# Kernel tuning notes

Hardware: AMD Instinct MI355X
Metric: run time of the kernel (lower is better)

Reference implementation:

```python
import jax, jax.numpy as jnp
import numpy as np

NEG_SLOPE = 0.01  # torch LeakyReLU default
BN_EPS = 1e-5

def leaky_relu(x):
    return jnp.where(x >= 0, x, NEG_SLOPE * x)

def setup_inputs() -> dict:
    key = jax.random.key(0)
    kx, kw, k1w, k1b, k2w, k2b = jax.random.split(key, 6)
    B, S, d = 512, 256, 64
    H, E = 64, 8  # n_hidden_sets, n_elements
    X = jax.random.normal(kx, (B, S, d), dtype=jnp.float32)
    # Wc ~ U(-1, 1) per init_weights
    Wc = jax.random.uniform(kw, (d, H * E), dtype=jnp.float32, minval=-1.0, maxval=1.0)
    # Linear layers: torch default init ~ U(-1/sqrt(fan_in), 1/sqrt(fan_in))
    b1 = 1.0 / np.sqrt(H)
    fc1_w = jax.random.uniform(k1w, (32, H), dtype=jnp.float32, minval=-b1, maxval=b1)
    fc1_b = jax.random.uniform(k1b, (32,), dtype=jnp.float32, minval=-b1, maxval=b1)
    b2 = 1.0 / np.sqrt(32)
    fc2_w = jax.random.uniform(k2w, (1, 32), dtype=jnp.float32, minval=-b2, maxval=b2)
    fc2_b = jax.random.uniform(jax.random.fold_in(key, 7), (1,), dtype=jnp.float32, minval=-b2, maxval=b2)
    gamma = jnp.ones((32,), dtype=jnp.float32)
    beta = jnp.zeros((32,), dtype=jnp.float32)
    return {"X": X, "Wc": Wc, "fc1_w": fc1_w, "fc1_b": fc1_b,
            "gamma": gamma, "beta": beta, "fc2_w": fc2_w, "fc2_b": fc2_b}

def reference(X, Wc, fc1_w, fc1_b, gamma, beta, fc2_w, fc2_b):
    B, S, d = X.shape
    HE = Wc.shape[1]
    H = fc1_w.shape[1]          # n_hidden_sets
    E = HE // H                 # n_elements
    # [B,S,d] @ [d,H*E] -> [B,S,H*E], LeakyReLU epilogue
    t = leaky_relu(jnp.matmul(X, Wc))
    # torch .view: row-major reshape to [B,S,E,H]
    t = t.reshape(B, S, E, H)
    t = jnp.max(t, axis=2)      # max over elements -> [B,S,H]
    t = jnp.sum(t, axis=1)      # sum over set -> [B,H]
    # fc1
    t = t @ fc1_w.T + fc1_b     # [B,32]
    # BatchNorm1d, training-mode batch statistics (biased var)
    mu = jnp.mean(t, axis=0)
    var = jnp.mean(jnp.square(t - mu), axis=0)
    t = (t - mu) * jax.lax.rsqrt(var + BN_EPS) * gamma + beta
    t = leaky_relu(t)
    out = t @ fc2_w.T + fc2_b   # [B,1]
    return out[:, 0]
```

## Files before the change

kernel.cpp:

```cpp
#include <hip/hip_runtime.h>

typedef __bf16 bf16x4 __attribute__((ext_vector_type(4)));
typedef __bf16 bf16x8 __attribute__((ext_vector_type(8)));
typedef float  f32x4  __attribute__((ext_vector_type(4)));

#define XS 68

__global__ __launch_bounds__(256, 2)
void fused_main(const float* __restrict__ X, const float* __restrict__ Wc,
                const float* __restrict__ fc1_w, const float* __restrict__ fc1_b,
                float* __restrict__ out1)
{
    __shared__ __bf16 xlds[64 * XS];
    __shared__ float  t0row[64];

    const int tid  = threadIdx.x;
    const int b    = blockIdx.x;
    const int wave = tid >> 6;
    const int lane = tid & 63;
    const int n    = lane & 15;
    const int q    = lane >> 4;

    const float4* xg = (const float4*)(X + (size_t)b * 256 * 64);

    float4 xv[4];
    #pragma unroll
    for (int i = 0; i < 4; ++i) xv[i] = xg[tid + i * 256];

    bf16x8 bf0[8], bf1[8];
    {
        const float* wbase = Wc + (q * 8) * 512 + wave * 16 + n;
        #pragma unroll
        for (int e = 0; e < 8; ++e) {
            const float* p = wbase + e * 64;
            #pragma unroll
            for (int j = 0; j < 8; ++j) {
                bf0[e][j] = (__bf16)p[j * 512];
                bf1[e][j] = (__bf16)p[(j + 32) * 512];
            }
        }
    }

    float hsum = 0.0f;

    for (int st = 0; st < 4; ++st) {
        #pragma unroll
        for (int i = 0; i < 4; ++i) {
            const int p = tid + i * 256;
            bf16x4 o;
            o[0] = (__bf16)xv[i].x; o[1] = (__bf16)xv[i].y;
            o[2] = (__bf16)xv[i].z; o[3] = (__bf16)xv[i].w;
            const int r = p >> 4, ck = p & 15;
            *(bf16x4*)&xlds[r * XS + ck * 4] = o;
        }
        __syncthreads();

        if (st < 3) {
            const float4* xgn = xg + (st + 1) * 1024;
            #pragma unroll
            for (int i = 0; i < 4; ++i) xv[i] = xgn[tid + i * 256];
        }

        bf16x8 a0[4], a1[4];
        #pragma unroll
        for (int t = 0; t < 4; ++t) {
            const int base = (t * 16 + n) * XS + q * 8;
            bf16x4 p0 = *(const bf16x4*)&xlds[base];
            bf16x4 p1 = *(const bf16x4*)&xlds[base + 4];
            bf16x4 p2 = *(const bf16x4*)&xlds[base + 32];
            bf16x4 p3 = *(const bf16x4*)&xlds[base + 36];
            a0[t] = __builtin_shufflevector(p0, p1, 0, 1, 2, 3, 4, 5, 6, 7);
            a1[t] = __builtin_shufflevector(p2, p3, 0, 1, 2, 3, 4, 5, 6, 7);
        }

        float rmax[4][4];
        #pragma unroll
        for (int t = 0; t < 4; ++t)
            #pragma unroll
            for (int r4 = 0; r4 < 4; ++r4) rmax[t][r4] = -3.0e38f;

        #pragma unroll
        for (int e = 0; e < 8; ++e) {
            #pragma unroll
            for (int t = 0; t < 4; ++t) {
                f32x4 acc = {0.f, 0.f, 0.f, 0.f};
                acc = __builtin_amdgcn_mfma_f32_16x16x32_bf16(a0[t], bf0[e], acc, 0, 0, 0);
                acc = __builtin_amdgcn_mfma_f32_16x16x32_bf16(a1[t], bf1[e], acc, 0, 0, 0);
                #pragma unroll
                for (int r4 = 0; r4 < 4; ++r4) {
                    rmax[t][r4] = fmaxf(rmax[t][r4], fmaxf(acc[r4], 0.01f * acc[r4]));
                }
            }
        }

        float s = 0.f;
        #pragma unroll
        for (int t = 0; t < 4; ++t)
            #pragma unroll
            for (int r4 = 0; r4 < 4; ++r4) s += rmax[t][r4];
        s += __shfl_xor(s, 16);
        s += __shfl_xor(s, 32);
        hsum += s;
        __syncthreads();
    }

    if (lane < 16) t0row[wave * 16 + lane] = hsum;
    __syncthreads();

    if (wave == 0) {
        const int j = lane & 31, half = lane >> 5;
        float p = 0.f;
        #pragma unroll
        for (int i = 0; i < 32; ++i)
            p += t0row[half * 32 + i] * fc1_w[j * 64 + half * 32 + i];
        p += __shfl_xor(p, 32);
        if (half == 0) out1[b * 32 + j] = p + fc1_b[j];
    }
}

__global__ __launch_bounds__(512)
void bn_fc2(const float* __restrict__ out1, const float* __restrict__ gamma,
            const float* __restrict__ beta, const float* __restrict__ fc2_w,
            const float* __restrict__ fc2_b, float* __restrict__ out)
{
    __shared__ float psum[16][32];
    __shared__ float psumsq[16][32];
    __shared__ float sa[32], sc[32];

    const int tid = threadIdx.x;
    const int j   = tid & 31;
    const int sl  = tid >> 5;

    float s = 0.f, ss = 0.f;
    #pragma unroll
    for (int i = 0; i < 32; ++i) {
        float v = out1[(sl * 32 + i) * 32 + j];
        s  += v;
        ss += v * v;
    }
    psum[sl][j]   = s;
    psumsq[sl][j] = ss;
    __syncthreads();

    if (tid < 32) {
        float S = 0.f, SS = 0.f;
        #pragma unroll
        for (int i = 0; i < 16; ++i) { S += psum[i][tid]; SS += psumsq[i][tid]; }
        const float mu  = S * (1.0f / 512.0f);
        const float var = SS * (1.0f / 512.0f) - mu * mu;
        const float rs  = rsqrtf(var + 1e-5f);
        const float a   = rs * gamma[tid];
        sa[tid] = a;
        sc[tid] = beta[tid] - mu * a;
    }
    __syncthreads();

    float acc = 0.f;
    #pragma unroll
    for (int jj = 0; jj < 32; ++jj) {
        float v = out1[tid * 32 + jj];
        float y = v * sa[jj] + sc[jj];
        y = fmaxf(y, 0.01f * y);
        acc += y * fc2_w[jj];
    }
    out[tid] = acc + fc2_b[0];
}

extern "C" void kernel_launch(void* const* d_in, const int* in_sizes, int n_in,
                              void* d_out, int out_size, void* d_ws, size_t ws_size,
                              hipStream_t stream) {
    const float* X      = (const float*)d_in[0];
    const float* Wc     = (const float*)d_in[1];
    const float* fc1_w  = (const float*)d_in[2];
    const float* fc1_b  = (const float*)d_in[3];
    const float* gamma  = (const float*)d_in[4];
    const float* beta   = (const float*)d_in[5];
    const float* fc2_w  = (const float*)d_in[6];
    const float* fc2_b  = (const float*)d_in[7];

    float* out1 = (float*)d_ws;

    fused_main<<<512, 256, 0, stream>>>(X, Wc, fc1_w, fc1_b, out1);
    bn_fc2<<<1, 512, 0, stream>>>(out1, gamma, beta, fc2_w, fc2_b, (float*)d_out);
}
```

Measured before the change: 100.0 us.

## Fuse BN/fc2 into main kernel via last-block atomic and double-buffer X tiles

Merges the second BN+fc2 kernel into the main kernel: each block increments a global counter, and the last block to finish computes the batch statistics and the final output. The X staging buffer in LDS is double-buffered, with a two-stage register prefetch, so one barrier per step is removed. A hipMemsetAsync is added to reset the counter, which replaces one kernel launch with a memset node. The tail work now runs on a single 256-thread block instead of 512 threads.

```diff
diff --git a/kernel.cpp b/kernel.cpp
--- a/kernel.cpp
+++ b/kernel.cpp
@@ -7,12 +7,19 @@
 #define XS 68
 
 __global__ __launch_bounds__(256, 2)
-void fused_main(const float* __restrict__ X, const float* __restrict__ Wc,
-                const float* __restrict__ fc1_w, const float* __restrict__ fc1_b,
-                float* __restrict__ out1)
+void fused_all(const float* __restrict__ X, const float* __restrict__ Wc,
+               const float* __restrict__ fc1_w, const float* __restrict__ fc1_b,
+               const float* __restrict__ gamma, const float* __restrict__ beta,
+               const float* __restrict__ fc2_w, const float* __restrict__ fc2_b,
+               float* __restrict__ out1, unsigned* __restrict__ cnt,
+               float* __restrict__ out)
 {
-    __shared__ __bf16 xlds[64 * XS];
+    __shared__ __bf16 xlds[2][64 * XS];
     __shared__ float  t0row[64];
+    __shared__ float  redsum[8][32];
+    __shared__ float  redsq[8][32];
+    __shared__ float  sa[32], sc[32];
+    __shared__ int    lastflag;
 
     const int tid  = threadIdx.x;
     const int b    = blockIdx.x;
@@ -23,9 +30,11 @@
 
     const float4* xg = (const float4*)(X + (size_t)b * 256 * 64);
 
-    float4 xv[4];
-    #pragma unroll
-    for (int i = 0; i < 4; ++i) xv[i] = xg[tid + i * 256];
+    float4 xv[2][4];
+    #pragma unroll
+    for (int i = 0; i < 4; ++i) xv[0][i] = xg[tid + i * 256];
+    #pragma unroll
+    for (int i = 0; i < 4; ++i) xv[1][i] = xg[1024 + tid + i * 256];
 
     bf16x8 bf0[8], bf1[8];
     {
@@ -43,32 +52,36 @@
 
     float hsum = 0.0f;
 
+    #pragma unroll
     for (int st = 0; st < 4; ++st) {
+        const int pbuf = st & 1;
+
         #pragma unroll
         for (int i = 0; i < 4; ++i) {
             const int p = tid + i * 256;
             bf16x4 o;
-            o[0] = (__bf16)xv[i].x; o[1] = (__bf16)xv[i].y;
-            o[2] = (__bf16)xv[i].z; o[3] = (__bf16)xv[i].w;
+            o[0] = (__bf16)xv[pbuf][i].x; o[1] = (__bf16)xv[pbuf][i].y;
+            o[2] = (__bf16)xv[pbuf][i].z; o[3] = (__bf16)xv[pbuf][i].w;
             const int r = p >> 4, ck = p & 15;
-            *(bf16x4*)&xlds[r * XS + ck * 4] = o;
-        }
+            *(bf16x4*)&xlds[pbuf][r * XS + ck * 4] = o;
+        }
+
+        if (st < 2) {
+            const float4* xgn = xg + (st + 2) * 1024;
+            #pragma unroll
+            for (int i = 0; i < 4; ++i) xv[pbuf][i] = xgn[tid + i * 256];
+        }
+
         __syncthreads();
-
-        if (st < 3) {
-            const float4* xgn = xg + (st + 1) * 1024;
-            #pragma unroll
-            for (int i = 0; i < 4; ++i) xv[i] = xgn[tid + i * 256];
-        }
 
         bf16x8 a0[4], a1[4];
         #pragma unroll
         for (int t = 0; t < 4; ++t) {
             const int base = (t * 16 + n) * XS + q * 8;
-            bf16x4 p0 = *(const bf16x4*)&xlds[base];
-            bf16x4 p1 = *(const bf16x4*)&xlds[base + 4];
-            bf16x4 p2 = *(const bf16x4*)&xlds[base + 32];
-            bf16x4 p3 = *(const bf16x4*)&xlds[base + 36];
+            bf16x4 p0 = *(const bf16x4*)&xlds[pbuf][base];
+            bf16x4 p1 = *(const bf16x4*)&xlds[pbuf][base + 4];
+            bf16x4 p2 = *(const bf16x4*)&xlds[pbuf][base + 32];
+            bf16x4 p3 = *(const bf16x4*)&xlds[pbuf][base + 36];
             a0[t] = __builtin_shufflevector(p0, p1, 0, 1, 2, 3, 4, 5, 6, 7);
             a1[t] = __builtin_shufflevector(p2, p3, 0, 1, 2, 3, 4, 5, 6, 7);
         }
@@ -101,7 +114,6 @@
         s += __shfl_xor(s, 16);
         s += __shfl_xor(s, 32);
         hsum += s;
-        __syncthreads();
     }
 
     if (lane < 16) t0row[wave * 16 + lane] = hsum;
@@ -116,36 +128,36 @@
         p += __shfl_xor(p, 32);
         if (half == 0) out1[b * 32 + j] = p + fc1_b[j];
     }
-}
-
-__global__ __launch_bounds__(512)
-void bn_fc2(const float* __restrict__ out1, const float* __restrict__ gamma,
-            const float* __restrict__ beta, const float* __restrict__ fc2_w,
-            const float* __restrict__ fc2_b, float* __restrict__ out)
-{
-    __shared__ float psum[16][32];
-    __shared__ float psumsq[16][32];
-    __shared__ float sa[32], sc[32];
-
-    const int tid = threadIdx.x;
-    const int j   = tid & 31;
-    const int sl  = tid >> 5;
-
+    __syncthreads();
+
+    if (tid == 0) {
+        __threadfence();
+        unsigned prev = __hip_atomic_fetch_add(cnt, 1u, __ATOMIC_ACQ_REL,
+                                               __HIP_MEMORY_SCOPE_AGENT);
+        lastflag = (prev == 511) ? 1 : 0;
+    }
+    __syncthreads();
+    if (!lastflag) return;
+
+    __threadfence();
+
+    const int j  = tid & 31;
+    const int sl = tid >> 5;
     float s = 0.f, ss = 0.f;
-    #pragma unroll
-    for (int i = 0; i < 32; ++i) {
-        float v = out1[(sl * 32 + i) * 32 + j];
+    #pragma unroll 8
+    for (int i = 0; i < 64; ++i) {
+        float v = out1[(sl * 64 + i) * 32 + j];
         s  += v;
         ss += v * v;
     }
-    psum[sl][j]   = s;
-    psumsq[sl][j] = ss;
+    redsum[sl][j] = s;
+    redsq[sl][j]  = ss;
     __syncthreads();
 
     if (tid < 32) {
         float S = 0.f, SS = 0.f;
         #pragma unroll
-        for (int i = 0; i < 16; ++i) { S += psum[i][tid]; SS += psumsq[i][tid]; }
+        for (int i = 0; i < 8; ++i) { S += redsum[i][tid]; SS += redsq[i][tid]; }
         const float mu  = S * (1.0f / 512.0f);
         const float var = SS * (1.0f / 512.0f) - mu * mu;
         const float rs  = rsqrtf(var + 1e-5f);
@@ -155,15 +167,19 @@
     }
     __syncthreads();
 
-    float acc = 0.f;
-    #pragma unroll
-    for (int jj = 0; jj < 32; ++jj) {
-        float v = out1[tid * 32 + jj];
-        float y = v * sa[jj] + sc[jj];
-        y = fmaxf(y, 0.01f * y);
-        acc += y * fc2_w[jj];
-    }
-    out[tid] = acc + fc2_b[0];
+    #pragma unroll
+    for (int r = 0; r < 2; ++r) {
+        const int row = tid * 2 + r;
+        float acc = 0.f;
+        #pragma unroll
+        for (int jj = 0; jj < 32; ++jj) {
+            float v = out1[row * 32 + jj];
+            float y = v * sa[jj] + sc[jj];
+            y = fmaxf(y, 0.01f * y);
+            acc += y * fc2_w[jj];
+        }
+        out[row] = acc + fc2_b[0];
+    }
 }
 
 extern "C" void kernel_launch(void* const* d_in, const int* in_sizes, int n_in,
@@ -178,8 +194,10 @@
     const float* fc2_w  = (const float*)d_in[6];
     const float* fc2_b  = (const float*)d_in[7];
 
-    float* out1 = (float*)d_ws;
-
-    fused_main<<<512, 256, 0, stream>>>(X, Wc, fc1_w, fc1_b, out1);
-    bn_fc2<<<1, 512, 0, stream>>>(out1, gamma, beta, fc2_w, fc2_b, (float*)d_out);
+    float*    out1 = (float*)d_ws;
+    unsigned* cnt  = (unsigned*)((char*)d_ws + 64 * 1024);
+
+    hipMemsetAsync(cnt, 0, sizeof(unsigned), stream);
+    fused_all<<<512, 256, 0, stream>>>(X, Wc, fc1_w, fc1_b, gamma, beta,
+                                       fc2_w, fc2_b, out1, cnt, (float*)d_out);
 }
```

Measured after the change: 113.9 us. +13.9%, slower.
